# Kernel optimization log

Hardware: AMD Instinct MI355X
Metric: run time of the kernel (lower is better)

Reference implementation:

```python
import jax, jax.numpy as jnp
import numpy as np

FS = 2  # dilated kernel size
DILS = tuple(2 ** i for _ in range(2) for i in range(10))  # 2 blocks x 10 layers
LWS = tuple((FS - 1) * d for d in DILS)  # left-wing shrink of each dilated conv
TOTAL_LW = sum(LWS)  # 2046


def _conv(x, w, dil=1):
    # x: (B, Cin, T), w: (Cout, Cin, K), valid causal (left-wing) conv
    return jax.lax.conv_general_dilated(x, w, (1,), 'VALID', rhs_dilation=(dil,),
                                        dimension_numbers=('NCH', 'OIH', 'NCH'))


def _tconv(x, w, stride):
    # PyTorch ConvTranspose1d(n,n,k,stride,padding=k-stride): out_len = S*stride + stride - k
    wf = jnp.flip(w, -1).transpose(1, 0, 2)  # (in,out,k) -> (out,in,k), flipped taps
    return jax.lax.conv_general_dilated(x, wf, (1,), [(stride - 1, stride - 1)],
                                        lhs_dilation=(stride,),
                                        dimension_numbers=('NCH', 'OIH', 'NCH'))


def _wavenet(wav, lc_sparse, lc_conv_w, lc_conv_b, ups_w0, ups_b0, ups_w1, ups_b1,
             ups_w2, ups_b2, ups_w3, ups_b3, emb_w, emb_b, base_w, base_b,
             sig_w, sig_b, gate_w, gate_b, psig_w, pgate_w, skp_w, res_w,
             post1_w, post1_b, post2_w, post2_b, speaker_inds, jitter_index):
    # jitter local conditioning frames along time
    lc = jnp.take_along_axis(lc_sparse, jitter_index[:, None, :], axis=2)
    # post-jitter conv (kernel 3, valid)
    lc = _conv(lc, lc_conv_w) + lc_conv_b[:, None]
    # upsampling chain to audio rate
    for w, b, s in ((ups_w0, ups_b0, 5), (ups_w1, ups_b1, 4), (ups_w2, ups_b2, 4), (ups_w3, ups_b3, 4)):
        lc = _tconv(lc, w, s) + b[:, None]
    # global (speaker) conditioning: Linear applied to one-hot == column gather
    gc = emb_w[:, speaker_inds].T + emb_b  # (B, G)
    cond = jnp.concatenate(
        [lc, jnp.broadcast_to(gc[:, :, None], gc.shape + (lc.shape[2],))], axis=1)  # (B, I+G, T0)
    # base 1x1 conv onto residual channels; wav already trimmed to T0 = cond length
    x = _conv(wav, base_w) + base_b[:, None]
    skp_sum = jnp.zeros(())
    cum = 0
    for i, (dil, lw) in enumerate(zip(DILS, LWS)):
        cl = cum + lw                      # cond lead aligning cond to this layer's output
        c = cond[:, :, cl:]
        filt = _conv(x, sig_w[i], dil) + sig_b[i][:, None] + _conv(c, psig_w[i])
        gate = _conv(x, gate_w[i], dil) + gate_b[i][:, None] + _conv(c, pgate_w[i])
        z = jnp.tanh(filt) * jax.nn.sigmoid(gate)
        sl = TOTAL_LW - cl                 # skip lead aligning z to final output length
        skp_sum = skp_sum + _conv(z[:, :, sl:], skp_w[i])
        x = _conv(z, res_w[i]) + x[:, :, lw:]
        cum = cl
    h = jax.nn.relu(skp_sum)
    h = jax.nn.relu(_conv(h, post1_w) + post1_b[:, None])
    h = _conv(h, post2_w) + post2_b[:, None]
    return jax.nn.log_softmax(h, axis=1)  # (B, n_quant, T_final)


def setup_inputs() -> dict:
    key = jax.random.key(0)
    ks = iter(jax.random.split(key, 64))
    B, S = 4, 64
    NLC_IN, NLC_OUT, NSPK, NGE = 64, 128, 40, 128
    NQ, NR, ND, NS, NP = 256, 384, 256, 256, 512
    NCOND = NLC_OUT + NGE
    L = 20
    T = 18308  # (((64-2)*5+5-25)*4+4-16)... upsampled cond length == wav length

    def rn(shape, scale=0.05):
        return jax.random.normal(next(ks), shape, jnp.float32) * scale

    return dict(
        wav=rn((B, NQ, T), 1.0),
        lc_sparse=rn((B, NLC_IN, S), 1.0),
        lc_conv_w=rn((NLC_OUT, NLC_IN, 3)), lc_conv_b=rn((NLC_OUT,)),
        ups_w0=rn((NLC_OUT, NLC_OUT, 25)), ups_b0=rn((NLC_OUT,)),
        ups_w1=rn((NLC_OUT, NLC_OUT, 16)), ups_b1=rn((NLC_OUT,)),
        ups_w2=rn((NLC_OUT, NLC_OUT, 16)), ups_b2=rn((NLC_OUT,)),
        ups_w3=rn((NLC_OUT, NLC_OUT, 16)), ups_b3=rn((NLC_OUT,)),
        emb_w=rn((NGE, NSPK)), emb_b=rn((NGE,)),
        base_w=rn((NR, NQ, 1)), base_b=rn((NR,)),
        sig_w=rn((L, ND, NR, FS)), sig_b=rn((L, ND)),
        gate_w=rn((L, ND, NR, FS)), gate_b=rn((L, ND)),
        psig_w=rn((L, ND, NCOND, 1)), pgate_w=rn((L, ND, NCOND, 1)),
        skp_w=rn((L, NS, ND, 1)), res_w=rn((L, NR, ND, 1)),
        post1_w=rn((NP, NS, 1)), post1_b=rn((NP,)),
        post2_w=rn((NQ, NP, 1)), post2_b=rn((NQ,)),
        speaker_inds=jax.random.randint(next(ks), (B,), 0, NSPK),
        jitter_index=jax.random.randint(next(ks), (B, S), 0, S),
    )


def reference(wav, lc_sparse, lc_conv_w, lc_conv_b, ups_w0, ups_b0, ups_w1, ups_b1,
              ups_w2, ups_b2, ups_w3, ups_b3, emb_w, emb_b, base_w, base_b,
              sig_w, sig_b, gate_w, gate_b, psig_w, pgate_w, skp_w, res_w,
              post1_w, post1_b, post2_w, post2_b, speaker_inds, jitter_index):
    return _wavenet(wav, lc_sparse, lc_conv_w, lc_conv_b, ups_w0, ups_b0, ups_w1, ups_b1,
                    ups_w2, ups_b2, ups_w3, ups_b3, emb_w, emb_b, base_w, base_b,
                    sig_w, sig_b, gate_w, gate_b, psig_w, pgate_w, skp_w, res_w,
                    post1_w, post1_b, post2_w, post2_b, speaker_inds, jitter_index)
```

## Files before the change

kernel.cpp:

```cpp
#include <hip/hip_runtime.h>
#include <hip/hip_bf16.h>
#include <math.h>


#define T_IN 18308
#define T_OUT 16262

typedef unsigned short u16;
typedef unsigned int u32;
typedef __attribute__((ext_vector_type(8))) short short8_t;
typedef __attribute__((ext_vector_type(4))) float f32x4;

__device__ __forceinline__ float bf2f(u16 h) { return __uint_as_float(((u32)h) << 16); }
__device__ __forceinline__ u16 f2bf(float f) {
  u32 u = __float_as_uint(f);
  return (u16)((u + 0x7fffu + ((u >> 16) & 1u)) >> 16);
}

__global__ void k_pack_frag(const float* __restrict__ src, u16* __restrict__ dst,
                            int M, int K, int L, long src_lstride) {
  int nks = K >> 5;
  long per = (long)M * K;
  long total = per * L;
  for (long idx = blockIdx.x * (long)blockDim.x + threadIdx.x; idx < total; idx += (long)gridDim.x * blockDim.x) {
    int l = (int)(idx / per); long r = idx - (long)l * per;
    int j = (int)(r & 7); int lane = (int)((r >> 3) & 63); int fid = (int)(r >> 9);
    int ks = fid % nks; int mt = fid / nks;
    int row = mt * 16 + (lane & 15);
    int col = ks * 32 + ((lane >> 4) << 3) + j;
    dst[idx] = f2bf(src[l * src_lstride + (long)row * K + col]);
  }
}

__global__ void k_pack_frag_gau(const float* __restrict__ sig_w, const float* __restrict__ gate_w,
                                const float* __restrict__ psig_w, const float* __restrict__ pgate_w,
                                u16* __restrict__ dstF, u16* __restrict__ dstG) {
  const long per = 229376;
  long total = per * 20;
  for (long idx = blockIdx.x * (long)blockDim.x + threadIdx.x; idx < total; idx += (long)gridDim.x * blockDim.x) {
    int l = (int)(idx / per); long r = idx - (long)l * per;
    int j = (int)(r & 7); int lane = (int)((r >> 3) & 63); int fid = (int)(r >> 9);
    int ks = fid % 28; int mt = fid / 28;
    int row = mt * 16 + (lane & 15);
    int k = ks * 32 + ((lane >> 4) << 3) + j;
    float vF, vG;
    if (k < 384) {
      vF = sig_w[(((long)l * 256 + row) * 384 + k) * 2 + 0];
      vG = gate_w[(((long)l * 256 + row) * 384 + k) * 2 + 0];
    } else if (k < 768) {
      vF = sig_w[(((long)l * 256 + row) * 384 + (k - 384)) * 2 + 1];
      vG = gate_w[(((long)l * 256 + row) * 384 + (k - 384)) * 2 + 1];
    } else {
      vF = psig_w[((long)l * 256 + row) * 256 + (k - 768)];
      vG = pgate_w[((long)l * 256 + row) * 256 + (k - 768)];
    }
    dstF[idx] = f2bf(vF);
    dstG[idx] = f2bf(vG);
  }
}

__global__ void k_pack_tconv(const float* __restrict__ w, float* __restrict__ dst,
                             int S, int K, int nk) {
  int Ktot = 128 * nk;
  long total = (long)S * Ktot * 128;
  for (long idx = blockIdx.x * (long)blockDim.x + threadIdx.x; idx < total; idx += (long)gridDim.x * blockDim.x) {
    int o = (int)(idx & 127);
    long tmp = idx >> 7;
    int k = (int)(tmp % Ktot);
    int p = (int)(tmp / Ktot);
    int i = k / nk, m = k % nk;
    dst[idx] = w[((long)i * 128 + o) * K + (K - 1 - (S - 1 - p) - m * S)];
  }
}

__global__ void k_pack_tc4f(const float* __restrict__ w, u16* __restrict__ dst) {
  const long perp = 65536;
  long total = perp * 4;
  for (long idx = blockIdx.x * (long)blockDim.x + threadIdx.x; idx < total; idx += (long)gridDim.x * blockDim.x) {
    int p = (int)(idx / perp); long r = idx - (long)p * perp;
    int j = (int)(r & 7); int lane = (int)((r >> 3) & 63); int fid = (int)(r >> 9);
    int ks = fid & 15; int mt = fid >> 4;
    int o = mt * 16 + (lane & 15);
    int k = ks * 32 + ((lane >> 4) << 3) + j;
    int i = k >> 2, m = k & 3;
    dst[idx] = f2bf(w[((long)i * 128 + o) * 16 + (12 + p - 4 * m)]);
  }
}

__global__ void k_im2col3(const float* __restrict__ lcs3, u16* __restrict__ dst) {
  long total = 4L * 4580 * 512;
  for (long idx = blockIdx.x * (long)blockDim.x + threadIdx.x; idx < total; idx += (long)gridDim.x * blockDim.x) {
    int col = (int)(idx & 511);
    long t2 = idx >> 9;
    int jj = (int)(t2 % 4580);
    int b = (int)(t2 / 4580);
    int i = col >> 2, m = col & 3;
    float v = (jj + m < 4580) ? lcs3[((long)b * 128 + i) * 4580 + jj + m] : 0.0f;
    dst[idx] = f2bf(v);
  }
}

__global__ void k_gc(const float* __restrict__ emb_w, const float* __restrict__ emb_b,
                     const int* __restrict__ spk, float* __restrict__ gc) {
  int i = threadIdx.x + blockIdx.x * blockDim.x;
  if (i < 512) { int b = i / 128, g = i % 128; gc[b * 128 + g] = emb_w[g * 40 + spk[b]] + emb_b[g]; }
}

__global__ void k_cbias(const float* __restrict__ psig_w, const float* __restrict__ pgate_w,
                        const float* __restrict__ sig_b, const float* __restrict__ gate_b,
                        const float* __restrict__ gc, float* __restrict__ cbias) {
  int l = blockIdx.x; int fg = blockIdx.y >> 2; int b = blockIdx.y & 3; int c = threadIdx.x;
  const float* p = fg ? pgate_w : psig_w;
  const float* bb = fg ? gate_b : sig_b;
  float acc = bb[l * 256 + c];
  const float* prow = p + ((long)(l * 256 + c)) * 256 + 128;
  const float* g = gc + b * 128;
  for (int k = 0; k < 128; ++k) acc += prow[k] * g[k];
  cbias[((l * 2 + fg) * 4 + b) * 256 + c] = acc;
}

__global__ void k_lc0(const float* __restrict__ lc_sparse, const int* __restrict__ jit,
                      const float* __restrict__ w, const float* __restrict__ bias, float* __restrict__ out) {
  int b = blockIdx.x; int t = blockIdx.y; int co = threadIdx.x;
  __shared__ float xs[64][3];
  for (int i = threadIdx.x; i < 192; i += blockDim.x) {
    int ci = i / 3, kk = i % 3;
    xs[ci][kk] = lc_sparse[((long)b * 64 + ci) * 64 + jit[b * 64 + t + kk]];
  }
  __syncthreads();
  float acc = bias[co];
  #pragma unroll 8
  for (int ci = 0; ci < 64; ++ci) {
    const float* wr = w + ((long)co * 64 + ci) * 3;
    acc += wr[0] * xs[ci][0] + wr[1] * xs[ci][1] + wr[2] * xs[ci][2];
  }
  out[((long)b * 128 + co) * 64 + t] = acc;
}

template<int NK>
__global__ __launch_bounds__(256) void k_tconvg(
    const float* __restrict__ xin, int Lin, int xstride,
    float* __restrict__ yout, int Lout, int ostride,
    const float* __restrict__ wp, const float* __restrict__ bias, int S) {
  const int Ktot = 128 * NK;
  __shared__ __align__(16) float Ws[32][64];
  __shared__ __align__(16) float Xs[32][64];
  int b = blockIdx.z;
  int p = blockIdx.y >> 1, bm0 = (blockIdx.y & 1) * 64;
  int j0 = blockIdx.x * 64;
  int tid = threadIdx.x, tn = tid & 15, tm = tid >> 4;
  float acc[4][4] = {};
  int kchunks = Ktot / 32;
  for (int kc = 0; kc < kchunks; ++kc) {
    int k0 = kc * 32;
    {
      int kk = tid >> 3, m8 = (tid & 7) * 8;
      const float* src = wp + ((long)p * Ktot + k0 + kk) * 128 + bm0 + m8;
      float4 f1 = *(const float4*)src;
      float4 f2 = *(const float4*)(src + 4);
      Ws[kk][m8 + 0] = f1.x; Ws[kk][m8 + 1] = f1.y; Ws[kk][m8 + 2] = f1.z; Ws[kk][m8 + 3] = f1.w;
      Ws[kk][m8 + 4] = f2.x; Ws[kk][m8 + 5] = f2.y; Ws[kk][m8 + 6] = f2.z; Ws[kk][m8 + 7] = f2.w;
    }
    #pragma unroll
    for (int rr = 0; rr < 8; ++rr) {
      int kk = rr * 4 + (tid >> 6), tt = tid & 63;
      int k = k0 + kk;
      int i = k / NK, m = k % NK;
      int j = j0 + tt;
      Xs[kk][tt] = (j + m < Lin) ? xin[((long)(b * 128 + i)) * xstride + j + m] : 0.0f;
    }
    __syncthreads();
    #pragma unroll 8
    for (int kk = 0; kk < 32; ++kk) {
      float av[4], bv[4];
      #pragma unroll
      for (int i = 0; i < 4; ++i) av[i] = Ws[kk][tm * 4 + i];
      #pragma unroll
      for (int j = 0; j < 4; ++j) bv[j] = Xs[kk][tn * 4 + j];
      #pragma unroll
      for (int i = 0; i < 4; ++i)
        #pragma unroll
        for (int j = 0; j < 4; ++j) acc[i][j] = fmaf(av[i], bv[j], acc[i][j]);
    }
    __syncthreads();
  }
  #pragma unroll
  for (int jj = 0; jj < 4; ++jj) {
    int j = j0 + tn * 4 + jj;
    int t = j * S + p;
    if (t >= Lout) continue;
    #pragma unroll
    for (int i = 0; i < 4; ++i) {
      int o = bm0 + tm * 4 + i;
      yout[((long)b * 128 + o) * ostride + t] = acc[i][jj] + bias[o];
    }
  }
}

__global__ __launch_bounds__(256) void k_tconv4m(
    const u16* __restrict__ im, const u16* __restrict__ Wp4,
    const float* __restrict__ bias, u16* __restrict__ out) {
  int lane = threadIdx.x & 63, wave = threadIdx.x >> 6;
  int b = blockIdx.z;
  int p = blockIdx.y >> 1, chb = (blockIdx.y & 1) << 6;
  int tbase = (blockIdx.x << 8) + (wave << 6);
  int lrow = lane & 15, lk = (lane >> 4) << 3;
  int mt0 = chb >> 4;
  const u16* Wp = Wp4 + (long)p * 65536;
  f32x4 zed = {0.f, 0.f, 0.f, 0.f};
  f32x4 acc[4][4];
  #pragma unroll
  for (int m = 0; m < 4; ++m)
    #pragma unroll
    for (int n = 0; n < 4; ++n) acc[m][n] = zed;
  const u16* ib = im + (long)b * 4580 * 512;
  for (int ks = 0; ks < 16; ++ks) {
    short8_t a[4];
    #pragma unroll
    for (int m = 0; m < 4; ++m)
      a[m] = *(const short8_t*)(Wp + ((long)((mt0 + m) * 16 + ks) << 9) + (lane << 3));
    #pragma unroll
    for (int n = 0; n < 4; ++n) {
      int j = tbase + (n << 4) + lrow;
      j = min(j, 4579);
      short8_t bv = *(const short8_t*)(ib + (long)j * 512 + (ks << 5) + lk);
      #pragma unroll
      for (int m = 0; m < 4; ++m)
        acc[m][n] = __builtin_amdgcn_mfma_f32_16x16x32_bf16(a[m], bv, acc[m][n], 0, 0, 0);
    }
  }
  #pragma unroll
  for (int n = 0; n < 4; ++n) {
    int j = tbase + (n << 4) + lrow;
    int t = j * 4 + p;
    if (t >= T_IN) continue;
    #pragma unroll
    for (int m = 0; m < 4; ++m) {
      int ch0 = chb + (m << 4) + ((lane >> 4) << 2);
      f32x4 bb = *(const f32x4*)(bias + ch0);
      ushort4 o;
      o.x = f2bf(acc[m][n][0] + bb[0]);
      o.y = f2bf(acc[m][n][1] + bb[1]);
      o.z = f2bf(acc[m][n][2] + bb[2]);
      o.w = f2bf(acc[m][n][3] + bb[3]);
      *(ushort4*)(out + ((long)b * T_IN + t) * 128 + ch0) = o;
    }
  }
}

__global__ __launch_bounds__(256) void k_wav_t(const float* __restrict__ wav, u16* __restrict__ dst) {
  __shared__ float xs[32][65];
  int b = blockIdx.z, c0 = blockIdx.y * 32, t0 = blockIdx.x * 64;
  int tid = threadIdx.x;
  #pragma unroll
  for (int i = 0; i < 8; ++i) {
    int idx = tid + i * 256;
    int c = idx >> 6, tl = idx & 63;
    int t = t0 + tl; if (t >= T_IN) t = T_IN - 1;
    xs[c][tl] = wav[((long)b * 256 + c0 + c) * T_IN + t];
  }
  __syncthreads();
  #pragma unroll
  for (int i = 0; i < 8; ++i) {
    int idx = tid + i * 256;
    int tl = idx >> 5, c = idx & 31;
    int t = t0 + tl;
    if (t < T_IN) dst[((long)b * T_IN + t) * 256 + c0 + c] = f2bf(xs[c][tl]);
  }
}

__global__ __launch_bounds__(256) void k_basem(
    const u16* __restrict__ wavT, const u16* __restrict__ Wp,
    const float* __restrict__ bias, u16* __restrict__ X) {
  int lane = threadIdx.x & 63, wave = threadIdx.x >> 6;
  int b = blockIdx.z, chb = blockIdx.y << 6;
  int tbase = (blockIdx.x << 8) + (wave << 6);
  int lrow = lane & 15, lk = (lane >> 4) << 3;
  int mt0 = chb >> 4;
  f32x4 zed = {0.f, 0.f, 0.f, 0.f};
  f32x4 acc[4][4];
  #pragma unroll
  for (int m = 0; m < 4; ++m)
    #pragma unroll
    for (int n = 0; n < 4; ++n) acc[m][n] = zed;
  const u16* xb = wavT + (long)b * T_IN * 256;
  for (int ks = 0; ks < 8; ++ks) {
    short8_t a[4];
    #pragma unroll
    for (int m = 0; m < 4; ++m)
      a[m] = *(const short8_t*)(Wp + ((long)((mt0 + m) * 8 + ks) << 9) + (lane << 3));
    #pragma unroll
    for (int n = 0; n < 4; ++n) {
      int row = tbase + (n << 4) + lrow;
      row = min(row, T_IN - 1);
      short8_t bv = *(const short8_t*)(xb + (long)row * 256 + (ks << 5) + lk);
      #pragma unroll
      for (int m = 0; m < 4; ++m)
        acc[m][n] = __builtin_amdgcn_mfma_f32_16x16x32_bf16(a[m], bv, acc[m][n], 0, 0, 0);
    }
  }
  #pragma unroll
  for (int n = 0; n < 4; ++n) {
    int t = tbase + (n << 4) + lrow;
    if (t >= T_IN) continue;
    #pragma unroll
    for (int m = 0; m < 4; ++m) {
      int ch0 = chb + (m << 4) + ((lane >> 4) << 2);
      f32x4 bb = *(const f32x4*)(bias + ch0);
      ushort4 o;
      o.x = f2bf(acc[m][n][0] + bb[0]);
      o.y = f2bf(acc[m][n][1] + bb[1]);
      o.z = f2bf(acc[m][n][2] + bb[2]);
      o.w = f2bf(acc[m][n][3] + bb[3]);
      *(ushort4*)(X + ((long)b * T_IN + t) * 384 + ch0) = o;
    }
  }
}

__global__ __launch_bounds__(256, 4) void k_gau4(
    const u16* __restrict__ Xc, const u16* __restrict__ Lc,
    const u16* __restrict__ WpF, const u16* __restrict__ WpG,
    const float* __restrict__ cb, u16* __restrict__ Z,
    int Lz, int d, int cl) {
  __shared__ __align__(16) u16 stg[2][2048];
  int lane = threadIdx.x & 63, wave = threadIdx.x >> 6;
  int tbase = blockIdx.y << 6;
  int b = blockIdx.z;
  int chb = (blockIdx.x << 7) + (wave << 5);
  int mt0 = chb >> 4;
  int lrow = lane & 15, lk16 = lane >> 4;
  const u16* xb = Xc + (long)b * T_IN * 384;
  const u16* lb = Lc + (long)b * T_IN * 128;
  const u16* pWF0 = WpF + (((long)mt0 * 28) << 9) + (lane << 3);
  const u16* pWF1 = WpF + (((long)(mt0 + 1) * 28) << 9) + (lane << 3);
  const u16* pWG0 = WpG + (((long)mt0 * 28) << 9) + (lane << 3);
  const u16* pWG1 = WpG + (((long)(mt0 + 1) * 28) << 9) + (lane << 3);
  int r0 = tbase + (wave << 4) + lrow;
  const u16* s0 = xb + (long)min(r0, T_IN - 1) * 384 + (lk16 << 3);
  const u16* s1 = xb + (long)min(r0 + d, T_IN - 1) * 384 + (lk16 << 3);
  const u16* s2 = lb + (long)min(r0 + cl, T_IN - 1) * 128 + (lk16 << 3);
  u16* wdst = &stg[0][0] + (wave << 9) + (lane << 3);

  f32x4 zed = {0.f, 0.f, 0.f, 0.f};
  f32x4 accF[2][4], accG[2][4];
  #pragma unroll
  for (int m = 0; m < 2; ++m)
    #pragma unroll
    for (int n = 0; n < 4; ++n) { accF[m][n] = zed; accG[m][n] = zed; }

  *(short8_t*)wdst = *(const short8_t*)s0;
  __syncthreads();
  #pragma unroll
  for (int ks = 0; ks < 28; ++ks) {
    short8_t nv;
    if (ks < 27) {
      int kn = ks + 1;
      const u16* sp = (kn < 12) ? (s0 + (kn << 5))
                    : (kn < 24) ? (s1 + ((kn - 12) << 5))
                                : (s2 + ((kn - 24) << 5));
      nv = *(const short8_t*)sp;
    }
    short8_t af0 = *(const short8_t*)(pWF0 + (ks << 9));
    short8_t af1 = *(const short8_t*)(pWF1 + (ks << 9));
    short8_t ag0 = *(const short8_t*)(pWG0 + (ks << 9));
    short8_t ag1 = *(const short8_t*)(pWG1 + (ks << 9));
    const u16* bufc = &stg[ks & 1][0];
    #pragma unroll
    for (int n = 0; n < 4; ++n) {
      short8_t bv = *(const short8_t*)(bufc + (n << 9) + (lane << 3));
      accF[0][n] = __builtin_amdgcn_mfma_f32_16x16x32_bf16(af0, bv, accF[0][n], 0, 0, 0);
      accF[1][n] = __builtin_amdgcn_mfma_f32_16x16x32_bf16(af1, bv, accF[1][n], 0, 0, 0);
      accG[0][n] = __builtin_amdgcn_mfma_f32_16x16x32_bf16(ag0, bv, accG[0][n], 0, 0, 0);
      accG[1][n] = __builtin_amdgcn_mfma_f32_16x16x32_bf16(ag1, bv, accG[1][n], 0, 0, 0);
    }
    if (ks < 27) *(short8_t*)(wdst + (((ks + 1) & 1) << 11)) = nv;
    __syncthreads();
  }

  const float* cbF = cb + b * 256;
  const float* cbG = cb + 1024 + b * 256;
  #pragma unroll
  for (int n = 0; n < 4; ++n) {
    int t = tbase + (n << 4) + lrow;
    if (t >= Lz) continue;
    #pragma unroll
    for (int m = 0; m < 2; ++m) {
      int ch0 = chb + (m << 4) + (lk16 << 2);
      f32x4 bf = *(const f32x4*)(cbF + ch0);
      f32x4 bg = *(const f32x4*)(cbG + ch0);
      ushort4 o;
      #pragma unroll
      for (int r = 0; r < 4; ++r) {
        float f = accF[m][n][r] + bf[r];
        float g = accG[m][n][r] + bg[r];
        f = fminf(fmaxf(f, -15.f), 15.f);
        float e2 = __expf(2.f * f);
        float th = 1.f - 2.f * __builtin_amdgcn_rcpf(e2 + 1.f);
        float sg = __builtin_amdgcn_rcpf(1.f + __expf(-g));
        u16 zz = f2bf(th * sg);
        if (r == 0) o.x = zz; else if (r == 1) o.y = zz; else if (r == 2) o.z = zz; else o.w = zz;
      }
      *(ushort4*)(Z + ((long)b * T_IN + t) * 256 + ch0) = o;
    }
  }
}

__global__ __launch_bounds__(256, 4) void k_skipres4(
    const u16* __restrict__ Zb, const u16* __restrict__ Wskp, const u16* __restrict__ Wres,
    const u16* __restrict__ Xres, float* __restrict__ skip, u16* __restrict__ Xout,
    int Lz, int sl, int lw, int first) {
  __shared__ __align__(16) u16 stg[2][2048];
  int lane = threadIdx.x & 63, wave = threadIdx.x >> 6;
  int slice = blockIdx.x;
  int tbase = blockIdx.y << 6;
  int b = blockIdx.z;
  bool issk = slice < 2;
  int mt0 = (issk ? slice * 8 : (slice - 2) * 8) + (wave << 1);
  const u16* Wp = issk ? Wskp : Wres;
  int lrow = lane & 15, lk16 = lane >> 4;
  const u16* pW0 = Wp + (((long)mt0 * 8) << 9) + (lane << 3);
  const u16* pW1 = Wp + (((long)(mt0 + 1) * 8) << 9) + (lane << 3);
  const u16* zb = Zb + (long)b * T_IN * 256;
  int r0 = min(tbase + (wave << 4) + lrow, T_IN - 1);
  const u16* sz = zb + (long)r0 * 256 + (lk16 << 3);
  u16* wdst = &stg[0][0] + (wave << 9) + (lane << 3);
  f32x4 zed = {0.f, 0.f, 0.f, 0.f};
  f32x4 acc[2][4];
  #pragma unroll
  for (int m = 0; m < 2; ++m)
    #pragma unroll
    for (int n = 0; n < 4; ++n) acc[m][n] = zed;

  *(short8_t*)wdst = *(const short8_t*)sz;
  __syncthreads();
  #pragma unroll
  for (int ks = 0; ks < 8; ++ks) {
    short8_t nv;
    if (ks < 7) nv = *(const short8_t*)(sz + ((ks + 1) << 5));
    short8_t a0 = *(const short8_t*)(pW0 + (ks << 9));
    short8_t a1 = *(const short8_t*)(pW1 + (ks << 9));
    const u16* bufc = &stg[ks & 1][0];
    #pragma unroll
    for (int n = 0; n < 4; ++n) {
      short8_t bv = *(const short8_t*)(bufc + (n << 9) + (lane << 3));
      acc[0][n] = __builtin_amdgcn_mfma_f32_16x16x32_bf16(a0, bv, acc[0][n], 0, 0, 0);
      acc[1][n] = __builtin_amdgcn_mfma_f32_16x16x32_bf16(a1, bv, acc[1][n], 0, 0, 0);
    }
    if (ks < 7) *(short8_t*)(wdst + (((ks + 1) & 1) << 11)) = nv;
    __syncthreads();
  }
  #pragma unroll
  for (int n = 0; n < 4; ++n) {
    int tg = tbase + (n << 4) + lrow;
    #pragma unroll
    for (int m = 0; m < 2; ++m) {
      int ch0 = ((mt0 + m) << 4) + (lk16 << 2);
      if (issk) {
        if (tg >= sl && tg < Lz) {
          float* p = skip + ((long)b * T_OUT + (tg - sl)) * 256 + ch0;
          if (first) { *(f32x4*)p = acc[m][n]; }
          else { f32x4 v = *(f32x4*)p; v += acc[m][n]; *(f32x4*)p = v; }
        }
      } else if (tg < Lz) {
        const u16* rp = Xres + ((long)b * T_IN + tg + lw) * 384 + ch0;
        ushort4 rv = *(const ushort4*)rp;
        ushort4 o;
        o.x = f2bf(acc[m][n][0] + bf2f(rv.x));
        o.y = f2bf(acc[m][n][1] + bf2f(rv.y));
        o.z = f2bf(acc[m][n][2] + bf2f(rv.z));
        o.w = f2bf(acc[m][n][3] + bf2f(rv.w));
        *(ushort4*)(Xout + ((long)b * T_IN + tg) * 384 + ch0) = o;
      }
    }
  }
}

__global__ __launch_bounds__(256) void k_post1(
    const float* __restrict__ skip, const u16* __restrict__ Wp,
    const float* __restrict__ b1, u16* __restrict__ h1) {
  int lane = threadIdx.x & 63, wave = threadIdx.x >> 6;
  int b = blockIdx.z, qb = blockIdx.y << 6;
  int tbase = (blockIdx.x << 8) + (wave << 6);
  int lrow = lane & 15, lk = (lane >> 4) << 3;
  int mt0 = qb >> 4;
  f32x4 zed = {0.f, 0.f, 0.f, 0.f};
  f32x4 acc[4][4];
  #pragma unroll
  for (int m = 0; m < 4; ++m)
    #pragma unroll
    for (int n = 0; n < 4; ++n) acc[m][n] = zed;
  const float* sb = skip + (long)b * T_OUT * 256;
  for (int ks = 0; ks < 8; ++ks) {
    short8_t a[4];
    #pragma unroll
    for (int m = 0; m < 4; ++m)
      a[m] = *(const short8_t*)(Wp + ((long)((mt0 + m) * 8 + ks) << 9) + (lane << 3));
    #pragma unroll
    for (int n = 0; n < 4; ++n) {
      int row = tbase + (n << 4) + lrow;
      row = min(row, T_OUT - 1);
      const float* src = sb + (long)row * 256 + (ks << 5) + lk;
      f32x4 v0 = *(const f32x4*)src;
      f32x4 v1 = *(const f32x4*)(src + 4);
      short8_t bv;
      #pragma unroll
      for (int j = 0; j < 4; ++j) bv[j] = (short)f2bf(fmaxf(v0[j], 0.f));
      #pragma unroll
      for (int j = 0; j < 4; ++j) bv[4 + j] = (short)f2bf(fmaxf(v1[j], 0.f));
      #pragma unroll
      for (int m = 0; m < 4; ++m)
        acc[m][n] = __builtin_amdgcn_mfma_f32_16x16x32_bf16(a[m], bv, acc[m][n], 0, 0, 0);
    }
  }
  #pragma unroll
  for (int n = 0; n < 4; ++n) {
    int t = tbase + (n << 4) + lrow;
    if (t >= T_OUT) continue;
    #pragma unroll
    for (int m = 0; m < 4; ++m) {
      int ch0 = qb + (m << 4) + ((lane >> 4) << 2);
      f32x4 bb = *(const f32x4*)(b1 + ch0);
      ushort4 o;
      o.x = f2bf(fmaxf(acc[m][n][0] + bb[0], 0.f));
      o.y = f2bf(fmaxf(acc[m][n][1] + bb[1], 0.f));
      o.z = f2bf(fmaxf(acc[m][n][2] + bb[2], 0.f));
      o.w = f2bf(fmaxf(acc[m][n][3] + bb[3], 0.f));
      *(ushort4*)(h1 + ((long)b * T_OUT + t) * 512 + ch0) = o;
    }
  }
}

__global__ __launch_bounds__(256) void k_post2sm(
    const u16* __restrict__ h1, const u16* __restrict__ Wp,
    const float* __restrict__ b2, float* __restrict__ out) {
  __shared__ float redM[4][64];
  __shared__ float redS[4][64];
  int lane = threadIdx.x & 63, wave = threadIdx.x >> 6;
  int b = blockIdx.z;
  int qb = wave << 6;
  int tb = blockIdx.x << 6;
  int lrow = lane & 15, lk = (lane >> 4) << 3;
  int mt0 = qb >> 4;
  f32x4 zed = {0.f, 0.f, 0.f, 0.f};
  f32x4 acc[4][4];
  #pragma unroll
  for (int m = 0; m < 4; ++m)
    #pragma unroll
    for (int n = 0; n < 4; ++n) acc[m][n] = zed;
  const u16* hb = h1 + (long)b * T_OUT * 512;
  for (int ks = 0; ks < 16; ++ks) {
    short8_t a[4];
    #pragma unroll
    for (int m = 0; m < 4; ++m)
      a[m] = *(const short8_t*)(Wp + ((long)((mt0 + m) * 16 + ks) << 9) + (lane << 3));
    #pragma unroll
    for (int n = 0; n < 4; ++n) {
      int row = tb + (n << 4) + lrow;
      row = min(row, T_OUT - 1);
      short8_t bv = *(const short8_t*)(hb + (long)row * 512 + (ks << 5) + lk);
      #pragma unroll
      for (int m = 0; m < 4; ++m)
        acc[m][n] = __builtin_amdgcn_mfma_f32_16x16x32_bf16(a[m], bv, acc[m][n], 0, 0, 0);
    }
  }
  #pragma unroll
  for (int m = 0; m < 4; ++m) {
    int q0 = qb + (m << 4) + ((lane >> 4) << 2);
    f32x4 bb = *(const f32x4*)(b2 + q0);
    #pragma unroll
    for (int n = 0; n < 4; ++n) acc[m][n] += bb;
  }
  float fm[4], fs[4];
  #pragma unroll
  for (int n = 0; n < 4; ++n) {
    float pm = -1e30f;
    #pragma unroll
    for (int m = 0; m < 4; ++m)
      #pragma unroll
      for (int r = 0; r < 4; ++r) pm = fmaxf(pm, acc[m][n][r]);
    pm = fmaxf(pm, __shfl_xor(pm, 16));
    pm = fmaxf(pm, __shfl_xor(pm, 32));
    if (lane < 16) redM[wave][(n << 4) + lane] = pm;
  }
  __syncthreads();
  #pragma unroll
  for (int n = 0; n < 4; ++n) {
    float mm = redM[0][(n << 4) + lrow];
    mm = fmaxf(mm, redM[1][(n << 4) + lrow]);
    mm = fmaxf(mm, redM[2][(n << 4) + lrow]);
    mm = fmaxf(mm, redM[3][(n << 4) + lrow]);
    fm[n] = mm;
    float ps = 0.f;
    #pragma unroll
    for (int m = 0; m < 4; ++m)
      #pragma unroll
      for (int r = 0; r < 4; ++r) ps += __expf(acc[m][n][r] - mm);
    ps += __shfl_xor(ps, 16);
    ps += __shfl_xor(ps, 32);
    if (lane < 16) redS[wave][(n << 4) + lane] = ps;
  }
  __syncthreads();
  #pragma unroll
  for (int n = 0; n < 4; ++n) {
    float ss = redS[0][(n << 4) + lrow] + redS[1][(n << 4) + lrow] +
               redS[2][(n << 4) + lrow] + redS[3][(n << 4) + lrow];
    fs[n] = fm[n] + logf(ss);
  }
  #pragma unroll
  for (int n = 0; n < 4; ++n) {
    int t = tb + (n << 4) + lrow;
    if (t >= T_OUT) continue;
    #pragma unroll
    for (int m = 0; m < 4; ++m) {
      int q0 = qb + (m << 4) + ((lane >> 4) << 2);
      #pragma unroll
      for (int r = 0; r < 4; ++r)
        out[((long)b * 256 + q0 + r) * T_OUT + t] = acc[m][n][r] - fs[n];
    }
  }
}

extern "C" void kernel_launch(void* const* d_in, const int* in_sizes, int n_in,
                              void* d_out, int out_size, void* d_ws, size_t ws_size,
                              hipStream_t stream) {
  const float* wav       = (const float*)d_in[0];
  const float* lc_sparse = (const float*)d_in[1];
  const float* lc_conv_w = (const float*)d_in[2];
  const float* lc_conv_b = (const float*)d_in[3];
  const float* ups_w[4]  = {(const float*)d_in[4], (const float*)d_in[6], (const float*)d_in[8], (const float*)d_in[10]};
  const float* ups_b[4]  = {(const float*)d_in[5], (const float*)d_in[7], (const float*)d_in[9], (const float*)d_in[11]};
  const float* emb_w     = (const float*)d_in[12];
  const float* emb_b     = (const float*)d_in[13];
  const float* base_w    = (const float*)d_in[14];
  const float* base_b    = (const float*)d_in[15];
  const float* sig_w     = (const float*)d_in[16];
  const float* sig_b     = (const float*)d_in[17];
  const float* gate_w    = (const float*)d_in[18];
  const float* gate_b    = (const float*)d_in[19];
  const float* psig_w    = (const float*)d_in[20];
  const float* pgate_w   = (const float*)d_in[21];
  const float* skp_w     = (const float*)d_in[22];
  const float* res_w     = (const float*)d_in[23];
  const float* post1_w   = (const float*)d_in[24];
  const float* post1_b   = (const float*)d_in[25];
  const float* post2_w   = (const float*)d_in[26];
  const float* post2_b   = (const float*)d_in[27];
  const int* spk         = (const int*)d_in[28];
  const int* jit         = (const int*)d_in[29];
  float* out = (float*)d_out;

  size_t off = 0;
  auto alloc = [&](size_t bytes) -> void* {
    off = (off + 255) & ~(size_t)255;
    void* p = (char*)d_ws + off;
    off += bytes;
    return p;
  };
  u16* wfgF   = (u16*)alloc(20L * 229376 * 2);
  u16* wfgG   = (u16*)alloc(20L * 229376 * 2);
  u16* wskpF  = (u16*)alloc(20L * 65536 * 2);
  u16* wresF  = (u16*)alloc(20L * 98304 * 2);
  u16* wbaseF = (u16*)alloc(384L * 256 * 2);
  u16* wp1F   = (u16*)alloc(512L * 256 * 2);
  u16* wp2F   = (u16*)alloc(256L * 512 * 2);
  float* wtc1 = (float*)alloc(5L * 640 * 128 * 4);
  float* wtc2 = (float*)alloc(4L * 512 * 128 * 4);
  float* wtc3 = (float*)alloc(4L * 512 * 128 * 4);
  u16* wtc4F  = (u16*)alloc(4L * 65536 * 2);
  float* cbias = (float*)alloc(20L * 2 * 4 * 256 * 4);
  float* gc    = (float*)alloc(4L * 128 * 4);
  u16* lcbf    = (u16*)alloc(4L * T_IN * 128 * 2);
  u16* xA      = (u16*)alloc(4L * T_IN * 384 * 2);
  u16* xB      = (u16*)alloc(4L * T_IN * 384 * 2);
  u16* zbuf    = (u16*)alloc(4L * T_IN * 256 * 2);
  float* skip  = (float*)alloc(4L * T_OUT * 256 * 4);
  float* lcs0 = (float*)zbuf;
  float* lcs1 = lcs0 + 4L * 128 * 64;
  float* lcs2 = lcs1 + 4L * 128 * 290;
  float* lcs3 = lcs2 + 4L * 128 * 1148;
  u16* im3    = xB;
  u16* wavT   = (u16*)skip;
  u16* h1bf   = xA;
  (void)ws_size; (void)in_sizes; (void)n_in; (void)out_size;

  k_pack_frag_gau<<<4480, 256, 0, stream>>>(sig_w, gate_w, psig_w, pgate_w, wfgF, wfgG);
  k_pack_frag<<<1280, 256, 0, stream>>>(skp_w, wskpF, 256, 256, 20, 256L * 256);
  k_pack_frag<<<1920, 256, 0, stream>>>(res_w, wresF, 384, 256, 20, 384L * 256);
  k_pack_frag<<<96, 256, 0, stream>>>(base_w, wbaseF, 384, 256, 1, 0);
  k_pack_frag<<<128, 256, 0, stream>>>(post1_w, wp1F, 512, 256, 1, 0);
  k_pack_frag<<<128, 256, 0, stream>>>(post2_w, wp2F, 256, 512, 1, 0);
  k_pack_tconv<<<320, 256, 0, stream>>>(ups_w[0], wtc1, 5, 25, 5);
  k_pack_tconv<<<256, 256, 0, stream>>>(ups_w[1], wtc2, 4, 16, 4);
  k_pack_tconv<<<256, 256, 0, stream>>>(ups_w[2], wtc3, 4, 16, 4);
  k_pack_tc4f<<<256, 256, 0, stream>>>(ups_w[3], wtc4F);
  k_gc<<<1, 512, 0, stream>>>(emb_w, emb_b, spk, gc);
  k_cbias<<<dim3(20, 8), 256, 0, stream>>>(psig_w, pgate_w, sig_b, gate_b, gc, cbias);

  k_lc0<<<dim3(4, 62), 128, 0, stream>>>(lc_sparse, jit, lc_conv_w, lc_conv_b, lcs0);
  k_tconvg<5><<<dim3(1, 10, 4), 256, 0, stream>>>(lcs0, 62, 64, lcs1, 290, 290, wtc1, ups_b[0], 5);
  k_tconvg<4><<<dim3(5, 8, 4), 256, 0, stream>>>(lcs1, 290, 290, lcs2, 1148, 1148, wtc2, ups_b[1], 4);
  k_tconvg<4><<<dim3(18, 8, 4), 256, 0, stream>>>(lcs2, 1148, 1148, lcs3, 4580, 4580, wtc3, ups_b[2], 4);
  k_im2col3<<<2048, 256, 0, stream>>>(lcs3, im3);
  k_tconv4m<<<dim3(18, 8, 4), 256, 0, stream>>>(im3, wtc4F, ups_b[3], lcbf);

  k_wav_t<<<dim3(287, 8, 4), 256, 0, stream>>>(wav, wavT);
  k_basem<<<dim3(72, 6, 4), 256, 0, stream>>>(wavT, wbaseF, base_b, xA);

  static const int DILS[20] = {1, 2, 4, 8, 16, 32, 64, 128, 256, 512,
                               1, 2, 4, 8, 16, 32, 64, 128, 256, 512};
  int cum = 0;
  u16* xc = xA; u16* xn = xB;
  for (int l = 0; l < 20; ++l) {
    int dd = DILS[l], lw = dd, cl = cum + lw;
    int Lz = T_IN - cl;
    int sl = 2046 - cl;
    int nt = (Lz + 63) / 64;
    k_gau4<<<dim3(2, nt, 4), 256, 0, stream>>>(
        xc, lcbf, wfgF + (long)l * 229376, wfgG + (long)l * 229376,
        cbias + (long)l * 2048, zbuf, Lz, dd, cl);
    int nsl = (l == 19) ? 2 : 5;
    k_skipres4<<<dim3(nsl, nt, 4), 256, 0, stream>>>(
        zbuf, wskpF + (long)l * 65536, wresF + (long)l * 98304,
        xc, skip, xn, Lz, sl, lw, (l == 0) ? 1 : 0);
    cum = cl;
    u16* t = xc; xc = xn; xn = t;
  }

  k_post1<<<dim3(64, 8, 4), 256, 0, stream>>>(skip, wp1F, post1_b, h1bf);
  k_post2sm<<<dim3(255, 1, 4), 256, 0, stream>>>(h1bf, wp2F, post2_b, out);
}
```

Before: 3.939 ms.

## Stage four K-steps per barrier in gate kernel, load whole Z tile upfront

The gated-activation kernel now stages four 32-wide K chunks into shared memory per iteration, cutting the barriers from 28 to 7 at the cost of 32KB of shared memory. Its grid is flattened and remapped so that each group of eight time tiles is visited by both channel halves back to back, which should improve cache reuse of the input rows. The skip/residual kernel loads the entire 256-channel Z tile into shared memory once and then runs all MFMA steps without any inner barriers. Launch bounds drop from 4 to 3 blocks per SIMD-group to make room for the larger shared footprint, which may reduce occupancy.

New measurement: 3.617 ms (median of 2 runs). 1.09x faster.

```diff
diff --git a/kernel.cpp b/kernel.cpp
--- a/kernel.cpp
+++ b/kernel.cpp
@@ -317,16 +317,20 @@
   }
 }
 
-__global__ __launch_bounds__(256, 4) void k_gau4(
+__global__ __launch_bounds__(256, 3) void k_gau6(
     const u16* __restrict__ Xc, const u16* __restrict__ Lc,
     const u16* __restrict__ WpF, const u16* __restrict__ WpG,
     const float* __restrict__ cb, u16* __restrict__ Z,
-    int Lz, int d, int cl) {
-  __shared__ __align__(16) u16 stg[2][2048];
+    int Lz, int d, int cl, int nt) {
+  __shared__ __align__(16) u16 stg[2][8192];
   int lane = threadIdx.x & 63, wave = threadIdx.x >> 6;
-  int tbase = blockIdx.y << 6;
+  int bx = blockIdx.x;
+  int tb = ((bx >> 4) << 3) + (bx & 7);
+  int chh = (bx >> 3) & 1;
+  if (tb >= nt) return;
+  int tbase = tb << 6;
   int b = blockIdx.z;
-  int chb = (blockIdx.x << 7) + (wave << 5);
+  int chb = (chh << 7) + (wave << 5);
   int mt0 = chb >> 4;
   int lrow = lane & 15, lk16 = lane >> 4;
   const u16* xb = Xc + (long)b * T_IN * 384;
@@ -339,7 +343,7 @@
   const u16* s0 = xb + (long)min(r0, T_IN - 1) * 384 + (lk16 << 3);
   const u16* s1 = xb + (long)min(r0 + d, T_IN - 1) * 384 + (lk16 << 3);
   const u16* s2 = lb + (long)min(r0 + cl, T_IN - 1) * 128 + (lk16 << 3);
-  u16* wdst = &stg[0][0] + (wave << 9) + (lane << 3);
+  u16* wd = &stg[0][0] + (wave << 9) + (lane << 3);
 
   f32x4 zed = {0.f, 0.f, 0.f, 0.f};
   f32x4 accF[2][4], accG[2][4];
@@ -348,32 +352,49 @@
     #pragma unroll
     for (int n = 0; n < 4; ++n) { accF[m][n] = zed; accG[m][n] = zed; }
 
-  *(short8_t*)wdst = *(const short8_t*)s0;
+  #pragma unroll
+  for (int j = 0; j < 4; ++j)
+    *(short8_t*)(wd + (j << 11)) = *(const short8_t*)(s0 + (j << 5));
   __syncthreads();
-  #pragma unroll
-  for (int ks = 0; ks < 28; ++ks) {
-    short8_t nv;
-    if (ks < 27) {
-      int kn = ks + 1;
-      const u16* sp = (kn < 12) ? (s0 + (kn << 5))
-                    : (kn < 24) ? (s1 + ((kn - 12) << 5))
-                                : (s2 + ((kn - 24) << 5));
-      nv = *(const short8_t*)sp;
-    }
-    short8_t af0 = *(const short8_t*)(pWF0 + (ks << 9));
-    short8_t af1 = *(const short8_t*)(pWF1 + (ks << 9));
-    short8_t ag0 = *(const short8_t*)(pWG0 + (ks << 9));
-    short8_t ag1 = *(const short8_t*)(pWG1 + (ks << 9));
-    const u16* bufc = &stg[ks & 1][0];
-    #pragma unroll
-    for (int n = 0; n < 4; ++n) {
-      short8_t bv = *(const short8_t*)(bufc + (n << 9) + (lane << 3));
-      accF[0][n] = __builtin_amdgcn_mfma_f32_16x16x32_bf16(af0, bv, accF[0][n], 0, 0, 0);
-      accF[1][n] = __builtin_amdgcn_mfma_f32_16x16x32_bf16(af1, bv, accF[1][n], 0, 0, 0);
-      accG[0][n] = __builtin_amdgcn_mfma_f32_16x16x32_bf16(ag0, bv, accG[0][n], 0, 0, 0);
-      accG[1][n] = __builtin_amdgcn_mfma_f32_16x16x32_bf16(ag1, bv, accG[1][n], 0, 0, 0);
-    }
-    if (ks < 27) *(short8_t*)(wdst + (((ks + 1) & 1) << 11)) = nv;
+
+  #pragma unroll
+  for (int ss = 0; ss < 7; ++ss) {
+    short8_t nv0, nv1, nv2, nv3;
+    if (ss < 6) {
+      int kb = ss * 4 + 4;
+      const u16* p0 = (kb + 0 < 12) ? (s0 + ((kb + 0) << 5)) : (kb + 0 < 24) ? (s1 + ((kb - 12) << 5)) : (s2 + ((kb - 24) << 5));
+      const u16* p1 = (kb + 1 < 12) ? (s0 + ((kb + 1) << 5)) : (kb + 1 < 24) ? (s1 + ((kb - 11) << 5)) : (s2 + ((kb - 23) << 5));
+      const u16* p2 = (kb + 2 < 12) ? (s0 + ((kb + 2) << 5)) : (kb + 2 < 24) ? (s1 + ((kb - 10) << 5)) : (s2 + ((kb - 22) << 5));
+      const u16* p3 = (kb + 3 < 12) ? (s0 + ((kb + 3) << 5)) : (kb + 3 < 24) ? (s1 + ((kb - 9) << 5)) : (s2 + ((kb - 21) << 5));
+      nv0 = *(const short8_t*)p0;
+      nv1 = *(const short8_t*)p1;
+      nv2 = *(const short8_t*)p2;
+      nv3 = *(const short8_t*)p3;
+    }
+    const u16* bufc = &stg[ss & 1][0];
+    #pragma unroll
+    for (int j = 0; j < 4; ++j) {
+      int ks = ss * 4 + j;
+      short8_t af0 = *(const short8_t*)(pWF0 + (ks << 9));
+      short8_t af1 = *(const short8_t*)(pWF1 + (ks << 9));
+      short8_t ag0 = *(const short8_t*)(pWG0 + (ks << 9));
+      short8_t ag1 = *(const short8_t*)(pWG1 + (ks << 9));
+      #pragma unroll
+      for (int n = 0; n < 4; ++n) {
+        short8_t bv = *(const short8_t*)(bufc + (j << 11) + (n << 9) + (lane << 3));
+        accF[0][n] = __builtin_amdgcn_mfma_f32_16x16x32_bf16(af0, bv, accF[0][n], 0, 0, 0);
+        accF[1][n] = __builtin_amdgcn_mfma_f32_16x16x32_bf16(af1, bv, accF[1][n], 0, 0, 0);
+        accG[0][n] = __builtin_amdgcn_mfma_f32_16x16x32_bf16(ag0, bv, accG[0][n], 0, 0, 0);
+        accG[1][n] = __builtin_amdgcn_mfma_f32_16x16x32_bf16(ag1, bv, accG[1][n], 0, 0, 0);
+      }
+    }
+    if (ss < 6) {
+      u16* wdn = wd + (((ss + 1) & 1) << 13);
+      *(short8_t*)(wdn + (0 << 11)) = nv0;
+      *(short8_t*)(wdn + (1 << 11)) = nv1;
+      *(short8_t*)(wdn + (2 << 11)) = nv2;
+      *(short8_t*)(wdn + (3 << 11)) = nv3;
+    }
     __syncthreads();
   }
 
@@ -405,11 +426,11 @@
   }
 }
 
-__global__ __launch_bounds__(256, 4) void k_skipres4(
+__global__ __launch_bounds__(256, 3) void k_skipres6(
     const u16* __restrict__ Zb, const u16* __restrict__ Wskp, const u16* __restrict__ Wres,
     const u16* __restrict__ Xres, float* __restrict__ skip, u16* __restrict__ Xout,
     int Lz, int sl, int lw, int first) {
-  __shared__ __align__(16) u16 stg[2][2048];
+  __shared__ __align__(16) u16 stg[16384];
   int lane = threadIdx.x & 63, wave = threadIdx.x >> 6;
   int slice = blockIdx.x;
   int tbase = blockIdx.y << 6;
@@ -423,7 +444,7 @@
   const u16* zb = Zb + (long)b * T_IN * 256;
   int r0 = min(tbase + (wave << 4) + lrow, T_IN - 1);
   const u16* sz = zb + (long)r0 * 256 + (lk16 << 3);
-  u16* wdst = &stg[0][0] + (wave << 9) + (lane << 3);
+  u16* wd = &stg[0] + (wave << 9) + (lane << 3);
   f32x4 zed = {0.f, 0.f, 0.f, 0.f};
   f32x4 acc[2][4];
   #pragma unroll
@@ -431,23 +452,21 @@
     #pragma unroll
     for (int n = 0; n < 4; ++n) acc[m][n] = zed;
 
-  *(short8_t*)wdst = *(const short8_t*)sz;
+  #pragma unroll
+  for (int j = 0; j < 8; ++j)
+    *(short8_t*)(wd + (j << 11)) = *(const short8_t*)(sz + (j << 5));
   __syncthreads();
+
   #pragma unroll
   for (int ks = 0; ks < 8; ++ks) {
-    short8_t nv;
-    if (ks < 7) nv = *(const short8_t*)(sz + ((ks + 1) << 5));
     short8_t a0 = *(const short8_t*)(pW0 + (ks << 9));
     short8_t a1 = *(const short8_t*)(pW1 + (ks << 9));
-    const u16* bufc = &stg[ks & 1][0];
     #pragma unroll
     for (int n = 0; n < 4; ++n) {
-      short8_t bv = *(const short8_t*)(bufc + (n << 9) + (lane << 3));
+      short8_t bv = *(const short8_t*)(&stg[0] + (ks << 11) + (n << 9) + (lane << 3));
       acc[0][n] = __builtin_amdgcn_mfma_f32_16x16x32_bf16(a0, bv, acc[0][n], 0, 0, 0);
       acc[1][n] = __builtin_amdgcn_mfma_f32_16x16x32_bf16(a1, bv, acc[1][n], 0, 0, 0);
     }
-    if (ks < 7) *(short8_t*)(wdst + (((ks + 1) & 1) << 11)) = nv;
-    __syncthreads();
   }
   #pragma unroll
   for (int n = 0; n < 4; ++n) {
@@ -715,11 +734,12 @@
     int Lz = T_IN - cl;
     int sl = 2046 - cl;
     int nt = (Lz + 63) / 64;
-    k_gau4<<<dim3(2, nt, 4), 256, 0, stream>>>(
+    int gx = 16 * ((nt + 7) >> 3);
+    k_gau6<<<dim3(gx, 1, 4), 256, 0, stream>>>(
         xc, lcbf, wfgF + (long)l * 229376, wfgG + (long)l * 229376,
-        cbias + (long)l * 2048, zbuf, Lz, dd, cl);
+        cbias + (long)l * 2048, zbuf, Lz, dd, cl, nt);
     int nsl = (l == 19) ? 2 : 5;
-    k_skipres4<<<dim3(nsl, nt, 4), 256, 0, stream>>>(
+    k_skipres6<<<dim3(nsl, nt, 4), 256, 0, stream>>>(
         zbuf, wskpF + (long)l * 65536, wresF + (long)l * 98304,
         xc, skip, xn, Lz, sl, lw, (l == 0) ? 1 : 0);
     cum = cl;
```
